# Kernel optimization log

Measured on AMD Instinct MI355X. Metric: run time of the kernel, lower is better.

The kernel has to match this reference:

```python
import jax, jax.numpy as jnp
import numpy as np

N = 50000       # nodes
E = 1600000     # edges (before self-loops)
H = 4           # heads
C = 32          # channels per head
G = 64          # graphs in batch
NEG_SLOPE = 0.2


def gat_conv(x, src, dst, W, att_src, att_dst, bias):
    # x: [N, Fin]; W: [Fin, H*C]; att_*: [H, C]; bias: [H*C]
    h = (x @ W).reshape(N, H, C)                       # [N, H, C]
    a_src = jnp.einsum('nhc,hc->nh', h, att_src)       # [N, H]
    a_dst = jnp.einsum('nhc,hc->nh', h, att_dst)       # [N, H]
    e = a_src[src] + a_dst[dst]                        # [E', H]
    e = jax.nn.leaky_relu(e, NEG_SLOPE)
    # softmax over incoming edges of each destination node
    m = jax.ops.segment_max(e, dst, num_segments=N)    # [N, H]
    ex = jnp.exp(e - m[dst])
    denom = jax.ops.segment_sum(ex, dst, num_segments=N)  # [N, H]
    alpha = ex / (denom[dst] + 1e-16)                  # [E', H]
    msg = h[src] * alpha[:, :, None]                   # [E', H, C]
    out = jax.ops.segment_sum(msg, dst, num_segments=N)  # [N, H, C]
    return out.reshape(N, H * C) + bias


def setup_inputs() -> dict:
    key = jax.random.key(0)
    ks = jax.random.split(key, 12)
    x = jax.random.normal(ks[0], (N, 128), dtype=jnp.float32)
    edge_index = jax.random.randint(ks[1], (2, E), 0, N, dtype=jnp.int64)
    batch = jnp.sort(jax.random.randint(ks[2], (N,), 0, G, dtype=jnp.int64))
    s = 0.05
    return {
        'x': x,
        'edge_index': edge_index,
        'batch': batch,
        'W1': jax.random.normal(ks[3], (128, H * C), dtype=jnp.float32) * s,
        'att_src1': jax.random.normal(ks[4], (H, C), dtype=jnp.float32) * s,
        'att_dst1': jax.random.normal(ks[5], (H, C), dtype=jnp.float32) * s,
        'b1': jnp.zeros((H * C,), dtype=jnp.float32),
        'W2': jax.random.normal(ks[6], (H * C, H * C), dtype=jnp.float32) * s,
        'att_src2': jax.random.normal(ks[7], (H, C), dtype=jnp.float32) * s,
        'att_dst2': jax.random.normal(ks[8], (H, C), dtype=jnp.float32) * s,
        'b2': jnp.zeros((H * C,), dtype=jnp.float32),
        'fc_W': jax.random.normal(ks[9], (H * C, 8), dtype=jnp.float32) * s,
        'fc_b': jnp.zeros((8,), dtype=jnp.float32),
    }


def reference(x, edge_index, batch, W1, att_src1, att_dst1, b1,
              W2, att_src2, att_dst2, b2, fc_W, fc_b):
    # add self loops (PyG GATConv default)
    ar = jnp.arange(N, dtype=edge_index.dtype)
    src = jnp.concatenate([edge_index[0], ar])
    dst = jnp.concatenate([edge_index[1], ar])
    h = gat_conv(x, src, dst, W1, att_src1, att_dst1, b1)
    h = jax.nn.elu(h)
    h = gat_conv(h, src, dst, W2, att_src2, att_dst2, b2)
    # global mean pool over graphs
    sums = jax.ops.segment_sum(h, batch, num_segments=G)          # [G, HC]
    cnt = jax.ops.segment_sum(jnp.ones((N,), h.dtype), batch, num_segments=G)
    pooled = sums / jnp.maximum(cnt, 1.0)[:, None]
    logits = pooled @ fc_W + fc_b                                  # [G, 8]
    return jax.nn.log_softmax(logits, axis=1)
```

## Files before the change

### kernel.cpp

```cpp
#include <hip/hip_runtime.h>
#include <math.h>

#define HC 128
#define GG 64
#define NEG 0.2f
#define TILE 4096
#define BW 128
#define SLOT 8192
#define LDA 136
#define GBS 32

typedef __attribute__((ext_vector_type(8))) short short8;
typedef __attribute__((ext_vector_type(4))) float floatx4;
typedef __attribute__((ext_vector_type(2))) float floatx2;

static __device__ __forceinline__ float leaky(float x) { return x > 0.f ? x : NEG * x; }

static __device__ __forceinline__ unsigned short f2bf(float f) {
    unsigned u = __float_as_uint(f);
    u += 0x7FFF + ((u >> 16) & 1);
    return (unsigned short)(u >> 16);
}

#if __has_builtin(__builtin_amdgcn_cvt_pk_f32_fp8) && __has_builtin(__builtin_amdgcn_cvt_pk_fp8_f32)
template <bool HI>
static __device__ __forceinline__ floatx2 fp8pair(unsigned int w) {
    return __builtin_amdgcn_cvt_pk_f32_fp8((int)w, HI);
}
static __device__ __forceinline__ unsigned int f32x2_fp8(float a, float b) {
    return ((unsigned int)__builtin_amdgcn_cvt_pk_fp8_f32(a, b, 0, false)) & 0xFFFFu;
}
#else
static __device__ __forceinline__ float fp8one(unsigned v) {
    unsigned e = (v >> 3) & 15u, m = v & 7u;
    float mag = e ? __uint_as_float(((e + 120u) << 23) | (m << 20))
                  : (float)m * 0.001953125f;
    return (v & 0x80u) ? -mag : mag;
}
template <bool HI>
static __device__ __forceinline__ floatx2 fp8pair(unsigned int w) {
    unsigned h = HI ? (w >> 16) : w;
    floatx2 r; r.x = fp8one(h & 0xFFu); r.y = fp8one((h >> 8) & 0xFFu);
    return r;
}
static __device__ __forceinline__ unsigned fp8enc(float f) {
    unsigned u = __float_as_uint(f);
    unsigned s = (u >> 24) & 0x80u;
    float a = fabsf(f);
    if (a >= 448.f) return s | 0x7Eu;
    if (a < 0.015625f) {
        unsigned m = (unsigned)(int)rintf(a * 512.f);
        return s | m;
    }
    u = __float_as_uint(a);
    u += 0xFFFFFu + ((u >> 20) & 1u);
    unsigned e8 = (u >> 23) - 120u;
    if (e8 >= 16u) return s | 0x7Eu;
    return s | (e8 << 3) | ((u >> 20) & 7u);
}
static __device__ __forceinline__ unsigned int f32x2_fp8(float a, float b) {
    return fp8enc(a) | (fp8enc(b) << 8);
}
#endif

static __device__ __forceinline__ void acc16(floatx2* acc, float w, const uint4& d) {
    floatx2 w2 = {w, w};
    acc[0] += w2 * fp8pair<false>(d.x);
    acc[1] += w2 * fp8pair<true>(d.x);
    acc[2] += w2 * fp8pair<false>(d.y);
    acc[3] += w2 * fp8pair<true>(d.y);
    acc[4] += w2 * fp8pair<false>(d.z);
    acc[5] += w2 * fp8pair<true>(d.z);
    acc[6] += w2 * fp8pair<false>(d.w);
    acc[7] += w2 * fp8pair<true>(d.w);
}

__global__ __launch_bounds__(256) void setup_k(const float* __restrict__ W1,
                                               const float* __restrict__ W2,
                                               unsigned short* __restrict__ Wt1,
                                               unsigned short* __restrict__ Wt2,
                                               int* __restrict__ gbcur,
                                               const int* __restrict__ batch,
                                               int* __restrict__ node_end,
                                               int* __restrict__ row_start,
                                               int NB, int Nn, int M) {
    int i = blockIdx.x * 256 + threadIdx.x;
    if (i < NB) gbcur[i * GBS] = i * SLOT;
    if (i == 0) row_start[Nn] = M;
    if (i < 32768) {
        const float* W = (i >> 14) ? W2 : W1;
        unsigned short* Wt = (i >> 14) ? Wt2 : Wt1;
        int d = i & 16383;
        int j = d & 7;
        int m = (d >> 3) & 15;
        int qf = d >> 7;
        int q = qf & 3;
        int f = qf >> 2;
        int kb = f & 3;
        int ct = f >> 2;
        int n = ct * 16 + m;
        int k = kb * 32 + q * 8 + j;
        Wt[d] = f2bf(W[k * 128 + n]);
    }
    if (i < Nn) {
        int b = batch[i];
        if (i == 0) {
            for (int g = 0; g < b; g++) node_end[g] = 0;
        }
        int bn = (i + 1 < Nn) ? batch[i + 1] : GG;
        for (int g = b; g < bn; g++) node_end[g] = i + 1;
    }
}

__global__ __launch_bounds__(512) void fused_k(const int* __restrict__ ei,
                                               int* __restrict__ gbcur,
                                               unsigned int* __restrict__ staging,
                                               int E, int M, int NB, int NBIN,
                                               const float* __restrict__ X,
                                               const unsigned short* __restrict__ Wt,
                                               const float* __restrict__ att_s,
                                               const float* __restrict__ att_d,
                                               unsigned char* __restrict__ H8,
                                               float* __restrict__ a_src,
                                               float* __restrict__ a_dst,
                                               int n_rows) {
    __shared__ __align__(16) char smem[34816];
    const int tid = threadIdx.x;

    if ((int)blockIdx.x < NBIN) {
        unsigned int* reorder = (unsigned int*)smem;
        int* s_cnt  = (int*)(smem + 16384);
        int* s_off  = (int*)(smem + 18432);
        int* s_run  = (int*)(smem + 20480);
        int* s_wsum = (int*)(smem + 22528);
        const int lane = tid & 63, wid = tid >> 6;
        const int tbase = blockIdx.x * TILE;
        const int tcnt = min(TILE, M - tbase);
        const bool fullLoad = (tbase + TILE <= E);
        const bool fullTile = (tcnt == TILE);

        unsigned int pk[8];
        if (fullLoad) {
            int s_[8], d_[8];
            #pragma unroll
            for (int q = 0; q < 8; q++) s_[q] = ei[tbase + tid + q * 512];
            #pragma unroll
            for (int q = 0; q < 8; q++) d_[q] = ei[E + tbase + tid + q * 512];
            #pragma unroll
            for (int q = 0; q < 8; q++)
                pk[q] = ((unsigned int)d_[q] << 16) | (unsigned int)s_[q];
        } else {
            #pragma unroll
            for (int q = 0; q < 8; q++) {
                int t = tid + q * 512;
                if (t < tcnt) {
                    int i = tbase + t;
                    int src, dst;
                    if (i < E) { src = ei[i]; dst = ei[E + i]; }
                    else       { src = dst = i - E; }
                    pk[q] = ((unsigned int)dst << 16) | (unsigned int)src;
                }
            }
        }

        for (int i = tid; i < NB; i += 512) s_cnt[i] = 0;
        __syncthreads();

        if (fullTile) {
            #pragma unroll
            for (int q = 0; q < 8; q++) atomicAdd(&s_cnt[pk[q] >> 23], 1);
        } else {
            #pragma unroll
            for (int q = 0; q < 8; q++) {
                int t = tid + q * 512;
                if (t < tcnt) atomicAdd(&s_cnt[pk[q] >> 23], 1);
            }
        }
        __syncthreads();

        {
            int v = (tid < NB) ? s_cnt[tid] : 0;
            int incl = v;
            #pragma unroll
            for (int off = 1; off < 64; off <<= 1) {
                int u = __shfl_up(incl, off);
                if (lane >= off) incl += u;
            }
            if (lane == 63) s_wsum[wid] = incl;
            __syncthreads();
            if (tid == 0) {
                int run = 0;
                #pragma unroll
                for (int w = 0; w < 8; w++) { int tv = s_wsum[w]; s_wsum[w] = run; run += tv; }
            }
            __syncthreads();
            int excl = s_wsum[wid] + incl - v;
            if (tid < NB) s_off[tid] = excl;
        }
        __syncthreads();

        for (int b = tid; b < NB; b += 512)
            s_run[b] = atomicAdd(&gbcur[b * GBS], s_cnt[b]);
        for (int b = tid; b < NB; b += 512) s_cnt[b] = s_off[b];
        __syncthreads();

        int rr[8];
        if (fullTile) {
            #pragma unroll
            for (int q = 0; q < 8; q++) rr[q] = atomicAdd(&s_cnt[pk[q] >> 23], 1);
            #pragma unroll
            for (int q = 0; q < 8; q++) reorder[rr[q]] = pk[q];
        } else {
            #pragma unroll
            for (int q = 0; q < 8; q++) {
                int t = tid + q * 512;
                if (t < tcnt) rr[q] = atomicAdd(&s_cnt[pk[q] >> 23], 1);
            }
            #pragma unroll
            for (int q = 0; q < 8; q++) {
                int t = tid + q * 512;
                if (t < tcnt) reorder[rr[q]] = pk[q];
            }
        }
        __syncthreads();

        if (fullTile) {
            unsigned int p[8];
            #pragma unroll
            for (int q = 0; q < 8; q++) p[q] = reorder[tid + q * 512];
            #pragma unroll
            for (int q = 0; q < 8; q++) {
                int t = tid + q * 512;
                int b = p[q] >> 23;
                staging[s_run[b] + (t - s_off[b])] = p[q];
            }
        } else {
            #pragma unroll
            for (int q = 0; q < 8; q++) {
                int t = tid + q * 512;
                if (t < tcnt) {
                    unsigned int p = reorder[t];
                    int b = p >> 23;
                    staging[s_run[b] + (t - s_off[b])] = p;
                }
            }
        }
    } else {
        unsigned short* As = (unsigned short*)smem;
        const int gb = blockIdx.x - NBIN;
        const int row0 = gb * 128;

        for (int i = tid; i < 4096; i += 512) {
            int r = i >> 5;
            int c4 = (i & 31) << 2;
            int gr = row0 + r;
            float4 v = (gr < n_rows) ? ((const float4*)&X[(size_t)gr * 128])[i & 31]
                                     : make_float4(0.f, 0.f, 0.f, 0.f);
            ushort4 bv = {f2bf(v.x), f2bf(v.y), f2bf(v.z), f2bf(v.w)};
            *(ushort4*)&As[r * LDA + c4] = bv;
        }
        __syncthreads();

        const int lane = tid & 63;
        const int wave = tid >> 6;
        const int m = lane & 15;
        const int quad = lane >> 4;
        const int wr = wave * 16;

        floatx4 acc[8];
        #pragma unroll
        for (int ct = 0; ct < 8; ct++) acc[ct] = (floatx4){0.f, 0.f, 0.f, 0.f};

        #pragma unroll
        for (int kb = 0; kb < 4; kb++) {
            short8 x0 = *(const short8*)&As[(wr + m) * LDA + kb * 32 + quad * 8];
            #pragma unroll
            for (int ct = 0; ct < 8; ct++) {
                short8 wf = *(const short8*)&Wt[(((ct * 4 + kb) * 4) + quad) * 128 + m * 8];
                acc[ct] = __builtin_amdgcn_mfma_f32_16x16x32_bf16(wf, x0, acc[ct], 0, 0, 0);
            }
        }

        const int q4 = quad * 4;
        int node = row0 + wr + m;
        bool vld = node < n_rows;
        float ps[4] = {0.f, 0.f, 0.f, 0.f};
        float pd[4] = {0.f, 0.f, 0.f, 0.f};
        #pragma unroll
        for (int ct = 0; ct < 8; ct++) {
            floatx4 v = acc[ct];
            int c0 = ct * 16 + q4;
            float4 avs = *(const float4*)&att_s[c0];
            float4 avd = *(const float4*)&att_d[c0];
            int h = ct >> 1;
            ps[h] += v[0] * avs.x + v[1] * avs.y + v[2] * avs.z + v[3] * avs.w;
            pd[h] += v[0] * avd.x + v[1] * avd.y + v[2] * avd.z + v[3] * avd.w;
            if (vld) {
                unsigned pk01 = f32x2_fp8(v[0], v[1]);
                unsigned pk23 = f32x2_fp8(v[2], v[3]);
                *(unsigned*)&H8[(size_t)node * 128 + c0] = pk01 | (pk23 << 16);
            }
        }
        #pragma unroll
        for (int h = 0; h < 4; h++) {
            ps[h] += __shfl_xor(ps[h], 16); ps[h] += __shfl_xor(ps[h], 32);
            pd[h] += __shfl_xor(pd[h], 16); pd[h] += __shfl_xor(pd[h], 32);
        }
        if (lane < 16 && vld) {
            float4 s4 = {ps[0], ps[1], ps[2], ps[3]};
            float4 d4 = {pd[0], pd[1], pd[2], pd[3]};
            *(float4*)&a_src[node * 4] = s4;
            *(float4*)&a_dst[node * 4] = d4;
        }
    }
}

__global__ __launch_bounds__(512) void unbin_k(const unsigned int* __restrict__ staging,
                                               const int* __restrict__ gbcur,
                                               int* __restrict__ row_start,
                                               unsigned short* __restrict__ srcs, int Nn) {
    __shared__ int s_cnt[BW];
    __shared__ int s_cur[BW];
    __shared__ int s_w[8];
    int b = blockIdx.x, t = threadIdx.x;
    int sbase = b * SLOT;
    int cnt = gbcur[b * GBS] - sbase;

    int pacc = 0;
    for (int i = t; i < b; i += 512) pacc += gbcur[i * GBS] - i * SLOT;
    #pragma unroll
    for (int off = 1; off < 64; off <<= 1) pacc += __shfl_xor(pacc, off);
    if ((t & 63) == 0) s_w[t >> 6] = pacc;
    __syncthreads();
    int bb = 0;
    #pragma unroll
    for (int w = 0; w < 8; w++) bb += s_w[w];
    __syncthreads();

    int n0 = b * BW;
    if (t < BW) s_cnt[t] = 0;
    __syncthreads();

    for (int j0 = t; j0 < cnt; j0 += 512 * 8) {
        unsigned int pk[8];
        if (j0 + 512 * 7 < cnt) {
            #pragma unroll
            for (int q = 0; q < 8; q++) pk[q] = staging[sbase + j0 + q * 512];
            #pragma unroll
            for (int q = 0; q < 8; q++) atomicAdd(&s_cnt[(pk[q] >> 16) & (BW - 1)], 1);
        } else {
            #pragma unroll
            for (int q = 0; q < 8; q++) {
                int j = j0 + q * 512;
                if (j < cnt) pk[q] = staging[sbase + j];
            }
            #pragma unroll
            for (int q = 0; q < 8; q++) {
                int j = j0 + q * 512;
                if (j < cnt) atomicAdd(&s_cnt[(pk[q] >> 16) & (BW - 1)], 1);
            }
        }
    }
    __syncthreads();
    int v = (t < BW) ? s_cnt[t] : 0;
    int incl = v;
    #pragma unroll
    for (int off = 1; off < 64; off <<= 1) {
        int u = __shfl_up(incl, off);
        if ((t & 63) >= off) incl += u;
    }
    if (t < BW && (t & 63) == 63) s_w[t >> 6] = incl;
    __syncthreads();
    int excl = incl - v + ((t >= 64 && t < BW) ? s_w[0] : 0);
    if (t < BW) {
        s_cur[t] = bb + excl;
        if (n0 + t < Nn) row_start[n0 + t] = bb + excl;
    }
    __syncthreads();

    for (int j0 = t; j0 < cnt; j0 += 512 * 8) {
        unsigned int pk[8];
        int rr[8];
        if (j0 + 512 * 7 < cnt) {
            #pragma unroll
            for (int q = 0; q < 8; q++) pk[q] = staging[sbase + j0 + q * 512];
            #pragma unroll
            for (int q = 0; q < 8; q++) rr[q] = atomicAdd(&s_cur[(pk[q] >> 16) & (BW - 1)], 1);
            #pragma unroll
            for (int q = 0; q < 8; q++) srcs[rr[q]] = (unsigned short)(pk[q] & 0xFFFFu);
        } else {
            #pragma unroll
            for (int q = 0; q < 8; q++) {
                int j = j0 + q * 512;
                if (j < cnt) pk[q] = staging[sbase + j];
            }
            #pragma unroll
            for (int q = 0; q < 8; q++) {
                int j = j0 + q * 512;
                if (j < cnt) rr[q] = atomicAdd(&s_cur[(pk[q] >> 16) & (BW - 1)], 1);
            }
            #pragma unroll
            for (int q = 0; q < 8; q++) {
                int j = j0 + q * 512;
                if (j < cnt) srcs[rr[q]] = (unsigned short)(pk[q] & 0xFFFFu);
            }
        }
    }
}

__global__ __launch_bounds__(128) void gemm_fused(const unsigned short* __restrict__ X,
                                                  const unsigned short* __restrict__ Wt,
                                                  const float* __restrict__ att_s,
                                                  const float* __restrict__ att_d,
                                                  unsigned char* __restrict__ H8,
                                                  float* __restrict__ a_src,
                                                  float* __restrict__ a_dst,
                                                  int n_rows) {
    __shared__ unsigned short As[64 * LDA];
    const int tid = threadIdx.x;
    const int row0 = blockIdx.x * 64;

    for (int i = tid; i < 1024; i += 128) {
        int r = i >> 4;
        int c8 = (i & 15) << 3;
        int gr = row0 + r;
        uint4 v = (gr < n_rows) ? *(const uint4*)&X[(size_t)gr * 128 + c8]
                                : make_uint4(0, 0, 0, 0);
        *(uint4*)&As[r * LDA + c8] = v;
    }
    __syncthreads();

    const int lane = tid & 63;
    const int wave = tid >> 6;
    const int m = lane & 15;
    const int quad = lane >> 4;
    const int wr0 = wave * 32;

    floatx4 acc[2][8];
    #pragma unroll
    for (int nt = 0; nt < 2; nt++)
        #pragma unroll
        for (int ct = 0; ct < 8; ct++)
            acc[nt][ct] = (floatx4){0.f, 0.f, 0.f, 0.f};

    #pragma unroll
    for (int kb = 0; kb < 4; kb++) {
        short8 x0 = *(const short8*)&As[(wr0 + m) * LDA + kb * 32 + quad * 8];
        short8 x1 = *(const short8*)&As[(wr0 + 16 + m) * LDA + kb * 32 + quad * 8];
        #pragma unroll
        for (int ct = 0; ct < 8; ct++) {
            short8 wf = *(const short8*)&Wt[(((ct * 4 + kb) * 4) + quad) * 128 + m * 8];
            acc[0][ct] = __builtin_amdgcn_mfma_f32_16x16x32_bf16(wf, x0, acc[0][ct], 0, 0, 0);
            acc[1][ct] = __builtin_amdgcn_mfma_f32_16x16x32_bf16(wf, x1, acc[1][ct], 0, 0, 0);
        }
    }

    const int q4 = quad * 4;
    #pragma unroll
    for (int nt = 0; nt < 2; nt++) {
        int node = row0 + wr0 + nt * 16 + m;
        bool vld = node < n_rows;
        float ps[4] = {0.f, 0.f, 0.f, 0.f};
        float pd[4] = {0.f, 0.f, 0.f, 0.f};
        #pragma unroll
        for (int ct = 0; ct < 8; ct++) {
            floatx4 v = acc[nt][ct];
            int c0 = ct * 16 + q4;
            float4 avs = *(const float4*)&att_s[c0];
            float4 avd = *(const float4*)&att_d[c0];
            int h = ct >> 1;
            ps[h] += v[0] * avs.x + v[1] * avs.y + v[2] * avs.z + v[3] * avs.w;
            pd[h] += v[0] * avd.x + v[1] * avd.y + v[2] * avd.z + v[3] * avd.w;
            if (vld) {
                unsigned pk01 = f32x2_fp8(v[0], v[1]);
                unsigned pk23 = f32x2_fp8(v[2], v[3]);
                *(unsigned*)&H8[(size_t)node * 128 + c0] = pk01 | (pk23 << 16);
            }
        }
        #pragma unroll
        for (int h = 0; h < 4; h++) {
            ps[h] += __shfl_xor(ps[h], 16); ps[h] += __shfl_xor(ps[h], 32);
            pd[h] += __shfl_xor(pd[h], 16); pd[h] += __shfl_xor(pd[h], 32);
        }
        if (lane < 16 && vld) {
            float4 s4 = {ps[0], ps[1], ps[2], ps[3]};
            float4 d4 = {pd[0], pd[1], pd[2], pd[3]};
            *(float4*)&a_src[node * 4] = s4;
            *(float4*)&a_dst[node * 4] = d4;
        }
    }
}

__global__ __launch_bounds__(256) void gat_agg(const unsigned char* __restrict__ H8,
                                               const float* __restrict__ a_src,
                                               const float* __restrict__ a_dst,
                                               const int* __restrict__ row_start,
                                               const unsigned short* __restrict__ srcs,
                                               const float* __restrict__ bias,
                                               unsigned short* __restrict__ OUT,
                                               const int* __restrict__ batch,
                                               float* __restrict__ partial,
                                               int n_rows, int mode) {
    __shared__ float ls[32][128];
    __shared__ int sg[32];
    int n = (blockIdx.x * 256 + threadIdx.x) >> 3;
    int li = threadIdx.x & 7;
    int hd = li >> 1;
    bool vld = n < n_rows;

    float o[16];
    #pragma unroll
    for (int k = 0; k < 16; k++) o[k] = 0.f;

    if (vld) {
        int base = row_start[n];
        int end = row_start[n + 1];
        float adh = a_dst[n * 4 + hd];

        floatx2 acc[8];
        #pragma unroll
        for (int k = 0; k < 8; k++) acc[k] = (floatx2){0.f, 0.f};
        float wsum = 0.f;

        int j = base;
        int head_n = min(end - j, (4 - (base & 3)) & 3);
        for (int q = 0; q < head_n; q++, j++) {
            int s0 = srcs[j];
            float w0 = __expf(leaky(a_src[s0 * 4 + hd] + adh));
            uint4 d0 = *(const uint4*)&H8[(size_t)s0 * 128 + li * 16];
            acc16(acc, w0, d0);
            wsum += w0;
        }
        for (; j + 4 <= end; j += 4) {
            uint2 sv = *(const uint2*)&srcs[j];
            int s0 = sv.x & 0xFFFFu, s1 = sv.x >> 16;
            int s2 = sv.y & 0xFFFFu, s3 = sv.y >> 16;
            float a0 = a_src[s0 * 4 + hd];
            float a1 = a_src[s1 * 4 + hd];
            float a2 = a_src[s2 * 4 + hd];
            float a3 = a_src[s3 * 4 + hd];
            uint4 d0 = *(const uint4*)&H8[(size_t)s0 * 128 + li * 16];
            uint4 d1 = *(const uint4*)&H8[(size_t)s1 * 128 + li * 16];
            uint4 d2 = *(const uint4*)&H8[(size_t)s2 * 128 + li * 16];
            uint4 d3 = *(const uint4*)&H8[(size_t)s3 * 128 + li * 16];
            float w0 = __expf(leaky(a0 + adh));
            float w1 = __expf(leaky(a1 + adh));
            float w2 = __expf(leaky(a2 + adh));
            float w3 = __expf(leaky(a3 + adh));
            acc16(acc, w0, d0);
            acc16(acc, w1, d1);
            acc16(acc, w2, d2);
            acc16(acc, w3, d3);
            wsum += (w0 + w1) + (w2 + w3);
        }
        for (; j < end; j++) {
            int s0 = srcs[j];
            float w0 = __expf(leaky(a_src[s0 * 4 + hd] + adh));
            uint4 d0 = *(const uint4*)&H8[(size_t)s0 * 128 + li * 16];
            acc16(acc, w0, d0);
            wsum += w0;
        }

        float ih = 1.0f / (wsum + 1e-16f);
        #pragma unroll
        for (int k = 0; k < 8; k++) {
            float2 bv = *(const float2*)&bias[li * 16 + 2 * k];
            o[2 * k]     = acc[k].x * ih + bv.x;
            o[2 * k + 1] = acc[k].y * ih + bv.y;
        }
    }

    if (mode == 0) {
        if (vld) {
            #pragma unroll
            for (int k = 0; k < 16; k++) o[k] = o[k] > 0.f ? o[k] : __expf(o[k]) - 1.f;
            unsigned int pk[8];
            #pragma unroll
            for (int k = 0; k < 8; k++)
                pk[k] = ((unsigned)f2bf(o[2 * k + 1]) << 16) | (unsigned)f2bf(o[2 * k]);
            uint4 s0v = {pk[0], pk[1], pk[2], pk[3]};
            uint4 s1v = {pk[4], pk[5], pk[6], pk[7]};
            unsigned short* op = &OUT[(size_t)n * 128 + li * 16];
            *(uint4*)op = s0v;
            *(uint4*)(op + 8) = s1v;
        }
    } else {
        int nl = threadIdx.x >> 3;
        int n0b = blockIdx.x * 32;
        float* row = &ls[nl][li * 16];
        *(float4*)&row[0]  = (float4){o[0], o[1], o[2], o[3]};
        *(float4*)&row[4]  = (float4){o[4], o[5], o[6], o[7]};
        *(float4*)&row[8]  = (float4){o[8], o[9], o[10], o[11]};
        *(float4*)&row[12] = (float4){o[12], o[13], o[14], o[15]};
        if (li == 0) sg[nl] = vld ? min(batch[n] - batch[n0b], 3) : 0;
        __syncthreads();
        int t = threadIdx.x;
        if (t < 128) {
            float a0 = 0.f, a1 = 0.f, a2 = 0.f, a3 = 0.f;
            #pragma unroll 8
            for (int r = 0; r < 32; r++) {
                float v = ls[r][t];
                int gr = sg[r];
                a0 += (gr == 0) ? v : 0.f;
                a1 += (gr == 1) ? v : 0.f;
                a2 += (gr == 2) ? v : 0.f;
                a3 += (gr == 3) ? v : 0.f;
            }
            float* pp = &partial[(size_t)blockIdx.x * 4 * 128];
            pp[t] = a0;
            pp[128 + t] = a1;
            pp[256 + t] = a2;
            pp[384 + t] = a3;
        }
    }
}

__global__ __launch_bounds__(64) void head_k(const float* __restrict__ partial,
                                             const int* __restrict__ node_end,
                                             const int* __restrict__ batch,
                                             const float* __restrict__ fcW,
                                             const float* __restrict__ fcb,
                                             float* __restrict__ out, int n_rows) {
    __shared__ float p[128];
    __shared__ float lg[8];
    int g = blockIdx.x, t = threadIdx.x;
    int s = (g > 0) ? node_end[g - 1] : 0;
    int e = node_end[g];
    float cnt = fmaxf((float)(e - s), 1.0f);
    float v0 = 0.f, v1 = 0.f;
    if (e > s) {
        int b0 = s >> 5;
        int b1 = (e - 1) >> 5;
        for (int b = b0; b <= b1; b++) {
            int slot = g - batch[b * 32];
            if (slot < 0 || slot > 3) continue;
            const float* pp = &partial[((size_t)b * 4 + slot) * 128];
            v0 += pp[t];
            v1 += pp[64 + t];
        }
    }
    p[t] = v0 / cnt;
    p[t + 64] = v1 / cnt;
    __syncthreads();
    if (t < 8) {
        float sacc = fcb[t];
        for (int k = 0; k < 128; k++) sacc += p[k] * fcW[k * 8 + t];
        lg[t] = sacc;
    }
    __syncthreads();
    if (t == 0) {
        float m = lg[0];
        for (int j = 1; j < 8; j++) m = fmaxf(m, lg[j]);
        float se = 0.f;
        for (int j = 0; j < 8; j++) se += expf(lg[j] - m);
        float lse = logf(se) + m;
        for (int j = 0; j < 8; j++) out[g * 8 + j] = lg[j] - lse;
    }
}

extern "C" void kernel_launch(void* const* d_in, const int* in_sizes, int n_in,
                              void* d_out, int out_size, void* d_ws, size_t ws_size,
                              hipStream_t stream) {
    const float* x    = (const float*)d_in[0];
    const int*   ei   = (const int*)d_in[1];
    const int*   batch= (const int*)d_in[2];
    const float* W1   = (const float*)d_in[3];
    const float* as1  = (const float*)d_in[4];
    const float* ad1  = (const float*)d_in[5];
    const float* b1   = (const float*)d_in[6];
    const float* W2   = (const float*)d_in[7];
    const float* as2  = (const float*)d_in[8];
    const float* ad2  = (const float*)d_in[9];
    const float* b2   = (const float*)d_in[10];
    const float* fcW  = (const float*)d_in[11];
    const float* fcb  = (const float*)d_in[12];
    float* out = (float*)d_out;

    const int Nn = in_sizes[0] / HC;
    const int E  = in_sizes[1] / 2;
    const int M  = E + Nn;
    const int NB = (Nn + BW - 1) / BW;
    const int NBIN = (M + TILE - 1) / TILE;
    const int GB1 = (Nn + 127) / 128;
    const int GB2 = (Nn + 63) / 64;
    const int NBLK2 = (Nn + 31) / 32;

    char* ws = (char*)d_ws;
    size_t off = 0;
    auto alloc = [&](size_t bytes) -> char* {
        char* p = ws + off;
        off = (off + bytes + 255) & ~(size_t)255;
        return p;
    };
    size_t hB_bytes  = (size_t)Nn * HC * 2;
    size_t stg_bytes = (size_t)NB * SLOT * 4;
    char* hB_region = alloc(hB_bytes > stg_bytes ? hB_bytes : stg_bytes);
    unsigned short* hB      = (unsigned short*)hB_region;
    unsigned int*   staging = (unsigned int*)hB_region;
    unsigned char*  H8      = (unsigned char*)alloc((size_t)Nn * HC);
    float* asrc      = (float*)alloc((size_t)Nn * 4 * 4);
    float* adst      = (float*)alloc((size_t)Nn * 4 * 4);
    unsigned short* srcs = (unsigned short*)alloc((size_t)M * 2);
    int*   row_start = (int*)alloc((size_t)(Nn + 1) * 4);
    float* partial   = (float*)alloc((size_t)NBLK2 * 4 * HC * 4);
    int*   node_end  = (int*)alloc((size_t)GG * 4);
    int*   gbcur     = (int*)alloc((size_t)NB * GBS * 4);
    unsigned short* Wt1 = (unsigned short*)alloc(16384 * 2);
    unsigned short* Wt2 = (unsigned short*)alloc(16384 * 2);

    setup_k<<<(Nn + 255) / 256, 256, 0, stream>>>(W1, W2, Wt1, Wt2, gbcur, batch,
                                                  node_end, row_start, NB, Nn, M);
    fused_k<<<NBIN + GB1, 512, 0, stream>>>(ei, gbcur, staging, E, M, NB, NBIN,
                                            x, Wt1, as1, ad1, H8, asrc, adst, Nn);
    unbin_k<<<NB, 512, 0, stream>>>(staging, gbcur, row_start, srcs, Nn);
    gat_agg<<<NBLK2, 256, 0, stream>>>(H8, asrc, adst, row_start, srcs, b1, hB,
                                       batch, partial, Nn, 0);
    gemm_fused<<<GB2, 128, 0, stream>>>(hB, Wt2, as2, ad2, H8, asrc, adst, Nn);
    gat_agg<<<NBLK2, 256, 0, stream>>>(H8, asrc, adst, row_start, srcs, b2, hB,
                                       batch, partial, Nn, 1);
    head_k<<<GG, 64, 0, stream>>>(partial, node_end, batch, fcW, fcb, out, Nn);
}
```

Measured before the change: 238.8 us.

## Fuse layer-1 aggregation with layer-2 GEMM and double binning tile size

```diff
diff --git a/kernel.cpp b/kernel.cpp
--- a/kernel.cpp
+++ b/kernel.cpp
@@ -4,7 +4,7 @@
 #define HC 128
 #define GG 64
 #define NEG 0.2f
-#define TILE 4096
+#define TILE 8192
 #define BW 128
 #define SLOT 8192
 #define LDA 136
@@ -124,34 +124,34 @@
                                                float* __restrict__ a_src,
                                                float* __restrict__ a_dst,
                                                int n_rows) {
-    __shared__ __align__(16) char smem[34816];
+    __shared__ __align__(16) char smem[39040];
     const int tid = threadIdx.x;
 
     if ((int)blockIdx.x < NBIN) {
         unsigned int* reorder = (unsigned int*)smem;
-        int* s_cnt  = (int*)(smem + 16384);
-        int* s_off  = (int*)(smem + 18432);
-        int* s_run  = (int*)(smem + 20480);
-        int* s_wsum = (int*)(smem + 22528);
+        int* s_cnt  = (int*)(smem + 32768);
+        int* s_off  = (int*)(smem + 34816);
+        int* s_run  = (int*)(smem + 36864);
+        int* s_wsum = (int*)(smem + 38912);
         const int lane = tid & 63, wid = tid >> 6;
         const int tbase = blockIdx.x * TILE;
         const int tcnt = min(TILE, M - tbase);
         const bool fullLoad = (tbase + TILE <= E);
         const bool fullTile = (tcnt == TILE);
 
-        unsigned int pk[8];
+        unsigned int pk[16];
         if (fullLoad) {
-            int s_[8], d_[8];
-            #pragma unroll
-            for (int q = 0; q < 8; q++) s_[q] = ei[tbase + tid + q * 512];
-            #pragma unroll
-            for (int q = 0; q < 8; q++) d_[q] = ei[E + tbase + tid + q * 512];
-            #pragma unroll
-            for (int q = 0; q < 8; q++)
+            int s_[16], d_[16];
+            #pragma unroll
+            for (int q = 0; q < 16; q++) s_[q] = ei[tbase + tid + q * 512];
+            #pragma unroll
+            for (int q = 0; q < 16; q++) d_[q] = ei[E + tbase + tid + q * 512];
+            #pragma unroll
+            for (int q = 0; q < 16; q++)
                 pk[q] = ((unsigned int)d_[q] << 16) | (unsigned int)s_[q];
         } else {
             #pragma unroll
-            for (int q = 0; q < 8; q++) {
+            for (int q = 0; q < 16; q++) {
                 int t = tid + q * 512;
                 if (t < tcnt) {
                     int i = tbase + t;
@@ -168,10 +168,10 @@
 
         if (fullTile) {
             #pragma unroll
-            for (int q = 0; q < 8; q++) atomicAdd(&s_cnt[pk[q] >> 23], 1);
+            for (int q = 0; q < 16; q++) atomicAdd(&s_cnt[pk[q] >> 23], 1);
         } else {
             #pragma unroll
-            for (int q = 0; q < 8; q++) {
+            for (int q = 0; q < 16; q++) {
                 int t = tid + q * 512;
                 if (t < tcnt) atomicAdd(&s_cnt[pk[q] >> 23], 1);
             }
@@ -204,20 +204,20 @@
         for (int b = tid; b < NB; b += 512) s_cnt[b] = s_off[b];
         __syncthreads();
 
-        int rr[8];
+        int rr[16];
         if (fullTile) {
             #pragma unroll
-            for (int q = 0; q < 8; q++) rr[q] = atomicAdd(&s_cnt[pk[q] >> 23], 1);
-            #pragma unroll
-            for (int q = 0; q < 8; q++) reorder[rr[q]] = pk[q];
+            for (int q = 0; q < 16; q++) rr[q] = atomicAdd(&s_cnt[pk[q] >> 23], 1);
+            #pragma unroll
+            for (int q = 0; q < 16; q++) reorder[rr[q]] = pk[q];
         } else {
             #pragma unroll
-            for (int q = 0; q < 8; q++) {
+            for (int q = 0; q < 16; q++) {
                 int t = tid + q * 512;
                 if (t < tcnt) rr[q] = atomicAdd(&s_cnt[pk[q] >> 23], 1);
             }
             #pragma unroll
-            for (int q = 0; q < 8; q++) {
+            for (int q = 0; q < 16; q++) {
                 int t = tid + q * 512;
                 if (t < tcnt) reorder[rr[q]] = pk[q];
             }
@@ -225,18 +225,18 @@
         __syncthreads();
 
         if (fullTile) {
-            unsigned int p[8];
-            #pragma unroll
-            for (int q = 0; q < 8; q++) p[q] = reorder[tid + q * 512];
-            #pragma unroll
-            for (int q = 0; q < 8; q++) {
+            unsigned int p[16];
+            #pragma unroll
+            for (int q = 0; q < 16; q++) p[q] = reorder[tid + q * 512];
+            #pragma unroll
+            for (int q = 0; q < 16; q++) {
                 int t = tid + q * 512;
                 int b = p[q] >> 23;
                 staging[s_run[b] + (t - s_off[b])] = p[q];
             }
         } else {
             #pragma unroll
-            for (int q = 0; q < 8; q++) {
+            for (int q = 0; q < 16; q++) {
                 int t = tid + q * 512;
                 if (t < tcnt) {
                     unsigned int p = reorder[t];
@@ -408,99 +408,171 @@
     }
 }
 
-__global__ __launch_bounds__(128) void gemm_fused(const unsigned short* __restrict__ X,
-                                                  const unsigned short* __restrict__ Wt,
-                                                  const float* __restrict__ att_s,
-                                                  const float* __restrict__ att_d,
-                                                  unsigned char* __restrict__ H8,
-                                                  float* __restrict__ a_src,
-                                                  float* __restrict__ a_dst,
-                                                  int n_rows) {
+__global__ __launch_bounds__(512) void agg_gemm2_k(const unsigned char* __restrict__ H8,
+                                                   const float* __restrict__ a_src,
+                                                   const float* __restrict__ a_dst,
+                                                   const int* __restrict__ row_start,
+                                                   const unsigned short* __restrict__ srcs,
+                                                   const float* __restrict__ bias,
+                                                   const unsigned short* __restrict__ Wt,
+                                                   const float* __restrict__ att_s,
+                                                   const float* __restrict__ att_d,
+                                                   unsigned char* __restrict__ H8b,
+                                                   float* __restrict__ a_src2,
+                                                   float* __restrict__ a_dst2,
+                                                   int n_rows) {
     __shared__ unsigned short As[64 * LDA];
     const int tid = threadIdx.x;
     const int row0 = blockIdx.x * 64;
 
-    for (int i = tid; i < 1024; i += 128) {
-        int r = i >> 4;
-        int c8 = (i & 15) << 3;
-        int gr = row0 + r;
-        uint4 v = (gr < n_rows) ? *(const uint4*)&X[(size_t)gr * 128 + c8]
-                                : make_uint4(0, 0, 0, 0);
-        *(uint4*)&As[r * LDA + c8] = v;
-    }
-    __syncthreads();
-
-    const int lane = tid & 63;
-    const int wave = tid >> 6;
-    const int m = lane & 15;
-    const int quad = lane >> 4;
-    const int wr0 = wave * 32;
-
-    floatx4 acc[2][8];
-    #pragma unroll
-    for (int nt = 0; nt < 2; nt++)
-        #pragma unroll
-        for (int ct = 0; ct < 8; ct++)
-            acc[nt][ct] = (floatx4){0.f, 0.f, 0.f, 0.f};
-
-    #pragma unroll
-    for (int kb = 0; kb < 4; kb++) {
-        short8 x0 = *(const short8*)&As[(wr0 + m) * LDA + kb * 32 + quad * 8];
-        short8 x1 = *(const short8*)&As[(wr0 + 16 + m) * LDA + kb * 32 + quad * 8];
-        #pragma unroll
-        for (int ct = 0; ct < 8; ct++) {
-            short8 wf = *(const short8*)&Wt[(((ct * 4 + kb) * 4) + quad) * 128 + m * 8];
-            acc[0][ct] = __builtin_amdgcn_mfma_f32_16x16x32_bf16(wf, x0, acc[0][ct], 0, 0, 0);
-            acc[1][ct] = __builtin_amdgcn_mfma_f32_16x16x32_bf16(wf, x1, acc[1][ct], 0, 0, 0);
-        }
-    }
-
-    const int q4 = quad * 4;
-    #pragma unroll
-    for (int nt = 0; nt < 2; nt++) {
-        int node = row0 + wr0 + nt * 16 + m;
+    {
+        int r = tid >> 3;
+        int n = row0 + r;
+        int li = tid & 7;
+        int hd = li >> 1;
+        bool vld = n < n_rows;
+
+        float o[16];
+        #pragma unroll
+        for (int k = 0; k < 16; k++) o[k] = 0.f;
+
+        if (vld) {
+            int base = row_start[n];
+            int end = row_start[n + 1];
+            float adh = a_dst[n * 4 + hd];
+
+            floatx2 acc[8];
+            #pragma unroll
+            for (int k = 0; k < 8; k++) acc[k] = (floatx2){0.f, 0.f};
+            float wsum = 0.f;
+
+            int j = base;
+            int head_n = min(end - j, (4 - (base & 3)) & 3);
+            for (int q = 0; q < head_n; q++, j++) {
+                int s0 = srcs[j];
+                float w0 = __expf(leaky(a_src[s0 * 4 + hd] + adh));
+                uint4 d0 = *(const uint4*)&H8[(size_t)s0 * 128 + li * 16];
+                acc16(acc, w0, d0);
+                wsum += w0;
+            }
+            for (; j + 4 <= end; j += 4) {
+                uint2 sv = *(const uint2*)&srcs[j];
+                int s0 = sv.x & 0xFFFFu, s1 = sv.x >> 16;
+                int s2 = sv.y & 0xFFFFu, s3 = sv.y >> 16;
+                float a0 = a_src[s0 * 4 + hd];
+                float a1 = a_src[s1 * 4 + hd];
+                float a2 = a_src[s2 * 4 + hd];
+                float a3 = a_src[s3 * 4 + hd];
+                uint4 d0 = *(const uint4*)&H8[(size_t)s0 * 128 + li * 16];
+                uint4 d1 = *(const uint4*)&H8[(size_t)s1 * 128 + li * 16];
+                uint4 d2 = *(const uint4*)&H8[(size_t)s2 * 128 + li * 16];
+                uint4 d3 = *(const uint4*)&H8[(size_t)s3 * 128 + li * 16];
+                float w0 = __expf(leaky(a0 + adh));
+                float w1 = __expf(leaky(a1 + adh));
+                float w2 = __expf(leaky(a2 + adh));
+                float w3 = __expf(leaky(a3 + adh));
+                acc16(acc, w0, d0);
+                acc16(acc, w1, d1);
+                acc16(acc, w2, d2);
+                acc16(acc, w3, d3);
+                wsum += (w0 + w1) + (w2 + w3);
+            }
+            for (; j < end; j++) {
+                int s0 = srcs[j];
+                float w0 = __expf(leaky(a_src[s0 * 4 + hd] + adh));
+                uint4 d0 = *(const uint4*)&H8[(size_t)s0 * 128 + li * 16];
+                acc16(acc, w0, d0);
+                wsum += w0;
+            }
+
+            float ih = 1.0f / (wsum + 1e-16f);
+            #pragma unroll
+            for (int k = 0; k < 8; k++) {
+                float2 bv = *(const float2*)&bias[li * 16 + 2 * k];
+                o[2 * k]     = acc[k].x * ih + bv.x;
+                o[2 * k + 1] = acc[k].y * ih + bv.y;
+            }
+            #pragma unroll
+            for (int k = 0; k < 16; k++) o[k] = o[k] > 0.f ? o[k] : __expf(o[k]) - 1.f;
+        }
+
+        unsigned int pk2[8];
+        #pragma unroll
+        for (int k = 0; k < 8; k++)
+            pk2[k] = ((unsigned)f2bf(o[2 * k + 1]) << 16) | (unsigned)f2bf(o[2 * k]);
+        unsigned short* Ap = &As[r * LDA + li * 16];
+        *(uint4*)Ap       = make_uint4(pk2[0], pk2[1], pk2[2], pk2[3]);
+        *(uint4*)(Ap + 8) = make_uint4(pk2[4], pk2[5], pk2[6], pk2[7]);
+    }
+    __syncthreads();
+
+    {
+        const int lane = tid & 63;
+        const int wave = tid >> 6;
+        const int m = lane & 15;
+        const int quad = lane >> 4;
+        const int wr = (wave & 3) * 16;
+        const int ctb = (wave >> 2) * 4;
+
+        floatx4 acc[4];
+        #pragma unroll
+        for (int c = 0; c < 4; c++) acc[c] = (floatx4){0.f, 0.f, 0.f, 0.f};
+
+        #pragma unroll
+        for (int kb = 0; kb < 4; kb++) {
+            short8 x0 = *(const short8*)&As[(wr + m) * LDA + kb * 32 + quad * 8];
+            #pragma unroll
+            for (int c = 0; c < 4; c++) {
+                int ct = ctb + c;
+                short8 wf = *(const short8*)&Wt[(((ct * 4 + kb) * 4) + quad) * 128 + m * 8];
+                acc[c] = __builtin_amdgcn_mfma_f32_16x16x32_bf16(wf, x0, acc[c], 0, 0, 0);
+            }
+        }
+
+        const int q4 = quad * 4;
+        int node = row0 + wr + m;
         bool vld = node < n_rows;
-        float ps[4] = {0.f, 0.f, 0.f, 0.f};
-        float pd[4] = {0.f, 0.f, 0.f, 0.f};
-        #pragma unroll
-        for (int ct = 0; ct < 8; ct++) {
-            floatx4 v = acc[nt][ct];
+        float ps[2] = {0.f, 0.f};
+        float pd[2] = {0.f, 0.f};
+        #pragma unroll
+        for (int c = 0; c < 4; c++) {
+            floatx4 v = acc[c];
+            int ct = ctb + c;
             int c0 = ct * 16 + q4;
             float4 avs = *(const float4*)&att_s[c0];
             float4 avd = *(const float4*)&att_d[c0];
-            int h = ct >> 1;
+            int h = c >> 1;
             ps[h] += v[0] * avs.x + v[1] * avs.y + v[2] * avs.z + v[3] * avs.w;
             pd[h] += v[0] * avd.x + v[1] * avd.y + v[2] * avd.z + v[3] * avd.w;
             if (vld) {
                 unsigned pk01 = f32x2_fp8(v[0], v[1]);
                 unsigned pk23 = f32x2_fp8(v[2], v[3]);
-                *(unsigned*)&H8[(size_t)node * 128 + c0] = pk01 | (pk23 << 16);
-            }
-        }
-        #pragma unroll
-        for (int h = 0; h < 4; h++) {
+                *(unsigned*)&H8b[(size_t)node * 128 + c0] = pk01 | (pk23 << 16);
+            }
+        }
+        #pragma unroll
+        for (int h = 0; h < 2; h++) {
             ps[h] += __shfl_xor(ps[h], 16); ps[h] += __shfl_xor(ps[h], 32);
             pd[h] += __shfl_xor(pd[h], 16); pd[h] += __shfl_xor(pd[h], 32);
         }
         if (lane < 16 && vld) {
-            float4 s4 = {ps[0], ps[1], ps[2], ps[3]};
-            float4 d4 = {pd[0], pd[1], pd[2], pd[3]};
-            *(float4*)&a_src[node * 4] = s4;
-            *(float4*)&a_dst[node * 4] = d4;
-        }
-    }
-}
-
-__global__ __launch_bounds__(256) void gat_agg(const unsigned char* __restrict__ H8,
-                                               const float* __restrict__ a_src,
-                                               const float* __restrict__ a_dst,
-                                               const int* __restrict__ row_start,
-                                               const unsigned short* __restrict__ srcs,
-                                               const float* __restrict__ bias,
-                                               unsigned short* __restrict__ OUT,
-                                               const int* __restrict__ batch,
-                                               float* __restrict__ partial,
-                                               int n_rows, int mode) {
+            float2 s2 = {ps[0], ps[1]};
+            float2 d2 = {pd[0], pd[1]};
+            *(float2*)&a_src2[node * 4 + (ctb >> 1)] = s2;
+            *(float2*)&a_dst2[node * 4 + (ctb >> 1)] = d2;
+        }
+    }
+}
+
+__global__ __launch_bounds__(256) void gat_agg2(const unsigned char* __restrict__ H8,
+                                                const float* __restrict__ a_src,
+                                                const float* __restrict__ a_dst,
+                                                const int* __restrict__ row_start,
+                                                const unsigned short* __restrict__ srcs,
+                                                const float* __restrict__ bias,
+                                                const int* __restrict__ batch,
+                                                float* __restrict__ partial,
+                                                int n_rows) {
     __shared__ float ls[32][128];
     __shared__ int sg[32];
     int n = (blockIdx.x * 256 + threadIdx.x) >> 3;
@@ -570,48 +642,32 @@
         }
     }
 
-    if (mode == 0) {
-        if (vld) {
-            #pragma unroll
-            for (int k = 0; k < 16; k++) o[k] = o[k] > 0.f ? o[k] : __expf(o[k]) - 1.f;
-            unsigned int pk[8];
-            #pragma unroll
-            for (int k = 0; k < 8; k++)
-                pk[k] = ((unsigned)f2bf(o[2 * k + 1]) << 16) | (unsigned)f2bf(o[2 * k]);
-            uint4 s0v = {pk[0], pk[1], pk[2], pk[3]};
-            uint4 s1v = {pk[4], pk[5], pk[6], pk[7]};
-            unsigned short* op = &OUT[(size_t)n * 128 + li * 16];
-            *(uint4*)op = s0v;
-            *(uint4*)(op + 8) = s1v;
-        }
-    } else {
-        int nl = threadIdx.x >> 3;
-        int n0b = blockIdx.x * 32;
-        float* row = &ls[nl][li * 16];
-        *(float4*)&row[0]  = (float4){o[0], o[1], o[2], o[3]};
-        *(float4*)&row[4]  = (float4){o[4], o[5], o[6], o[7]};
-        *(float4*)&row[8]  = (float4){o[8], o[9], o[10], o[11]};
-        *(float4*)&row[12] = (float4){o[12], o[13], o[14], o[15]};
-        if (li == 0) sg[nl] = vld ? min(batch[n] - batch[n0b], 3) : 0;
-        __syncthreads();
-        int t = threadIdx.x;
-        if (t < 128) {
-            float a0 = 0.f, a1 = 0.f, a2 = 0.f, a3 = 0.f;
-            #pragma unroll 8
-            for (int r = 0; r < 32; r++) {
-                float v = ls[r][t];
-                int gr = sg[r];
-                a0 += (gr == 0) ? v : 0.f;
-                a1 += (gr == 1) ? v : 0.f;
-                a2 += (gr == 2) ? v : 0.f;
-                a3 += (gr == 3) ? v : 0.f;
-            }
-            float* pp = &partial[(size_t)blockIdx.x * 4 * 128];
-            pp[t] = a0;
-            pp[128 + t] = a1;
-            pp[256 + t] = a2;
-            pp[384 + t] = a3;
-        }
+    int nl = threadIdx.x >> 3;
+    int n0b = blockIdx.x * 32;
+    float* row = &ls[nl][li * 16];
+    *(float4*)&row[0]  = (float4){o[0], o[1], o[2], o[3]};
+    *(float4*)&row[4]  = (float4){o[4], o[5], o[6], o[7]};
+    *(float4*)&row[8]  = (float4){o[8], o[9], o[10], o[11]};
+    *(float4*)&row[12] = (float4){o[12], o[13], o[14], o[15]};
+    if (li == 0) sg[nl] = vld ? min(batch[n] - batch[n0b], 3) : 0;
+    __syncthreads();
+    int t = threadIdx.x;
+    if (t < 128) {
+        float a0 = 0.f, a1 = 0.f, a2 = 0.f, a3 = 0.f;
+        #pragma unroll 8
+        for (int r = 0; r < 32; r++) {
+            float v = ls[r][t];
+            int gr = sg[r];
+            a0 += (gr == 0) ? v : 0.f;
+            a1 += (gr == 1) ? v : 0.f;
+            a2 += (gr == 2) ? v : 0.f;
+            a3 += (gr == 3) ? v : 0.f;
+        }
+        float* pp = &partial[(size_t)blockIdx.x * 4 * 128];
+        pp[t] = a0;
+        pp[128 + t] = a1;
+        pp[256 + t] = a2;
+        pp[384 + t] = a3;
     }
 }
 
@@ -682,7 +738,7 @@
     const int NB = (Nn + BW - 1) / BW;
     const int NBIN = (M + TILE - 1) / TILE;
     const int GB1 = (Nn + 127) / 128;
-    const int GB2 = (Nn + 63) / 64;
+    const int AGB = (Nn + 63) / 64;
     const int NBLK2 = (Nn + 31) / 32;
 
     char* ws = (char*)d_ws;
@@ -692,14 +748,13 @@
         off = (off + bytes + 255) & ~(size_t)255;
         return p;
     };
-    size_t hB_bytes  = (size_t)Nn * HC * 2;
-    size_t stg_bytes = (size_t)NB * SLOT * 4;
-    char* hB_region = alloc(hB_bytes > stg_bytes ? hB_bytes : stg_bytes);
-    unsigned short* hB      = (unsigned short*)hB_region;
-    unsigned int*   staging = (unsigned int*)hB_region;
-    unsigned char*  H8      = (unsigned char*)alloc((size_t)Nn * HC);
+    unsigned int* staging = (unsigned int*)alloc((size_t)NB * SLOT * 4);
+    unsigned char* H8  = (unsigned char*)alloc((size_t)Nn * HC);
+    unsigned char* H8b = (unsigned char*)alloc((size_t)Nn * HC);
     float* asrc      = (float*)alloc((size_t)Nn * 4 * 4);
     float* adst      = (float*)alloc((size_t)Nn * 4 * 4);
+    float* asrc2     = (float*)alloc((size_t)Nn * 4 * 4);
+    float* adst2     = (float*)alloc((size_t)Nn * 4 * 4);
     unsigned short* srcs = (unsigned short*)alloc((size_t)M * 2);
     int*   row_start = (int*)alloc((size_t)(Nn + 1) * 4);
     float* partial   = (float*)alloc((size_t)NBLK2 * 4 * HC * 4);
@@ -713,10 +768,9 @@
     fused_k<<<NBIN + GB1, 512, 0, stream>>>(ei, gbcur, staging, E, M, NB, NBIN,
                                             x, Wt1, as1, ad1, H8, asrc, adst, Nn);
     unbin_k<<<NB, 512, 0, stream>>>(staging, gbcur, row_start, srcs, Nn);
-    gat_agg<<<NBLK2, 256, 0, stream>>>(H8, asrc, adst, row_start, srcs, b1, hB,
-                                       batch, partial, Nn, 0);
-    gemm_fused<<<GB2, 128, 0, stream>>>(hB, Wt2, as2, ad2, H8, asrc, adst, Nn);
-    gat_agg<<<NBLK2, 256, 0, stream>>>(H8, asrc, adst, row_start, srcs, b2, hB,
-                                       batch, partial, Nn, 1);
+    agg_gemm2_k<<<AGB, 512, 0, stream>>>(H8, asrc, adst, row_start, srcs, b1,
+                                         Wt2, as2, ad2, H8b, asrc2, adst2, Nn);
+    gat_agg2<<<NBLK2, 256, 0, stream>>>(H8b, asrc2, adst2, row_start, srcs, b2,
+                                        batch, partial, Nn);
     head_k<<<GG, 64, 0, stream>>>(partial, node_end, batch, fcW, fcb, out, Nn);
 }
```

Result: faster. 233.3 us (-2.3%).
